# Performance work log

Measured on AMD Instinct MI355X. Metric: run time of the kernel, lower is better.

Reference implementation:

```python
import jax, jax.numpy as jnp
import numpy as np

B, T = 32, 1024
TEMP_IN, STAT_IN = 128, 64
TEMP_OUT, STAT_OUT = 128, 64
EPS = 1e-5
NEG_SLOPE = 0.01


def _bn_eval(x, gamma, beta, mean, var):
    # BatchNorm1d in eval mode (running stats)
    return (x - mean) * jax.lax.rsqrt(var + EPS) * gamma + beta


def _leaky_relu(x):
    return jnp.where(x >= 0, x, NEG_SLOPE * x)


def setup_inputs() -> dict:
    key = jax.random.key(0)
    k = jax.random.split(key, 6)
    # deterministic ragged lengths in [512, 1024]
    lengths_np = (512 + (np.arange(B) * 37) % 513).astype(np.int64)
    N = int(lengths_np.sum())  # 23450
    batch_idx = np.repeat(np.arange(B), lengths_np).astype(np.int32)
    pos_idx = np.concatenate([np.arange(l) for l in lengths_np]).astype(np.int32)
    valid = (np.arange(T)[None, :] < lengths_np[:, None])  # [B, T]
    mask_repeat = valid[:, :, None] & valid[:, None, :]    # [B, T, T]

    inp = {
        "x_temp": jax.random.normal(k[0], (N, TEMP_IN), jnp.float32),
        "x_stat": jax.random.normal(k[1], (B, STAT_IN), jnp.float32),
        "temp_attn": jax.random.normal(k[2], (B, T, T), jnp.float32) * 0.1,
        "mask_repeat": jnp.asarray(mask_repeat),
        "lengths": jnp.asarray(lengths_np),
        "batch_idx": jnp.asarray(batch_idx),
        "pos_idx": jnp.asarray(pos_idx),
        # non_linear_temp: Linear(TEMP_IN+STAT_IN -> TEMP_OUT) + BN
        "W1": jax.random.normal(k[3], (TEMP_OUT, TEMP_IN + STAT_IN), jnp.float32) / np.sqrt(TEMP_IN + STAT_IN),
        "b1": jnp.zeros((TEMP_OUT,), jnp.float32),
        "gamma1": jnp.ones((TEMP_OUT,), jnp.float32),
        "beta1": jnp.zeros((TEMP_OUT,), jnp.float32),
        "mean1": jnp.zeros((TEMP_OUT,), jnp.float32),
        "var1": jnp.ones((TEMP_OUT,), jnp.float32),
        # non_linear_stat: Linear(STAT_IN -> STAT_OUT) + BN
        "W2": jax.random.normal(k[4], (STAT_OUT, STAT_IN), jnp.float32) / np.sqrt(STAT_IN),
        "b2": jnp.zeros((STAT_OUT,), jnp.float32),
        "gamma2": jnp.ones((STAT_OUT,), jnp.float32),
        "beta2": jnp.zeros((STAT_OUT,), jnp.float32),
        "mean2": jnp.zeros((STAT_OUT,), jnp.float32),
        "var2": jnp.ones((STAT_OUT,), jnp.float32),
    }
    return inp


def reference(x_temp, x_stat, temp_attn, mask_repeat, lengths, batch_idx, pos_idx,
              W1, b1, gamma1, beta1, mean1, var1,
              W2, b2, gamma2, beta2, mean2, var2):
    # repeat_static_features: gather per-batch static feats to packed rows
    x_stat_rep = x_stat[batch_idx]                              # [N, STAT_IN]
    h = jnp.concatenate((x_temp, x_stat_rep), axis=-1) @ W1.T + b1
    h = _leaky_relu(_bn_eval(h, gamma1, beta1, mean1, var1))    # [N, TEMP_OUT]

    # pad_packed_sequences: scatter packed rows into [B, T, C] (zeros elsewhere)
    padded = jnp.zeros((B, T, TEMP_OUT), h.dtype).at[batch_idx, pos_idx].set(h)

    # self attention: softmax(x x^T / sqrt(d)) over padded rows (as original)
    d = jnp.asarray(TEMP_OUT, h.dtype)
    qk = jnp.einsum('btc,bsc->bts', padded, padded) / jnp.sqrt(d)
    self_attn = jax.nn.softmax(qk, axis=-1)

    attn = jnp.where(mask_repeat, self_attn + temp_attn, jnp.asarray(0.0, h.dtype))

    x_stat_out = _leaky_relu(_bn_eval(x_stat @ W2.T + b2, gamma2, beta2, mean2, var2))

    x_out_pad = jnp.einsum('bts,bsc->btc', attn, padded)        # [B, T, TEMP_OUT]
    # pack_padded_sequences: gather valid positions back to packed layout
    x_out = x_out_pad[batch_idx, pos_idx]                       # [N, TEMP_OUT]
    return (x_out, x_stat_out)
```

## Files before the change

kernel.cpp:

```cpp
#include <hip/hip_runtime.h>
#include <hip/hip_bf16.h>
#include <hip/hip_fp16.h>

typedef __hip_bfloat16 bf16;
typedef __attribute__((ext_vector_type(8))) short short8;
typedef __attribute__((ext_vector_type(4))) float f32x4;

#define EPS 1e-5f
#define NSLOPE 0.01f

__device__ __forceinline__ float b2f(bf16 v) { return __bfloat162float(v); }

__device__ __forceinline__ float ld1(const void* p, size_t idx, int isbf) {
  if (isbf) return b2f(((const bf16*)p)[idx]);
  return ((const float*)p)[idx];
}
__device__ __forceinline__ void st1(void* p, size_t idx, int isbf, float v) {
  if (isbf) ((bf16*)p)[idx] = __float2bfloat16(v);
  else      ((float*)p)[idx] = v;
}
__device__ __forceinline__ short f2bs(float x) {
  bf16 t = __float2bfloat16(x);
  short s; __builtin_memcpy(&s, &t, 2); return s;
}
__device__ __forceinline__ short8 pack8f(const float* p) {
  float4 a = *(const float4*)p, b = *(const float4*)(p + 4);
  short8 r;
  r[0] = f2bs(a.x); r[1] = f2bs(a.y); r[2] = f2bs(a.z); r[3] = f2bs(a.w);
  r[4] = f2bs(b.x); r[5] = f2bs(b.y); r[6] = f2bs(b.z); r[7] = f2bs(b.w);
  return r;
}

__global__ void meta_kernel(const void* __restrict__ xt,
                            const int* __restrict__ bidx, const int* __restrict__ pidx,
                            int N, int B, int* __restrict__ rs, int* __restrict__ ln,
                            int* __restrict__ flag,
                            const void* __restrict__ W1, bf16* __restrict__ w1b, int w1n) {
  int isbf_l = 0;
  {
    unsigned w = ((const unsigned*)xt)[threadIdx.x & 63];
    unsigned lo = w & 0xffffu;
    unsigned ex = (lo >> 7) & 0xffu;
    bool sane = ((lo & 0x7fffu) == 0u) || (ex >= 96u && ex <= 134u);
    unsigned long long m = __ballot(sane);
    isbf_l = (__popcll(m) >= 48) ? 1 : 0;
    if (blockIdx.x == 0 && threadIdx.x == 0) flag[0] = isbf_l;
  }
  int stride = gridDim.x * blockDim.x;
  int g0 = blockIdx.x * blockDim.x + threadIdx.x;
  for (int i = g0; i < N; i += stride) {
    int b = bidx[i];
    if ((unsigned)b >= (unsigned)B) continue;
    if (i == 0 || bidx[i - 1] != b) rs[b] = i;
    if (i == N - 1 || bidx[i + 1] != b) ln[b] = pidx[i] + 1;
  }
  for (int i = g0; i < w1n; i += stride) {
    int o = i / 192, k = i - o * 192;
    int ct = o >> 4, n = o & 15;
    int ks = k >> 5, rem = k & 31;
    int q = rem >> 3, j = rem & 7;
    int fi = ((ct * 6 + ks) * 64 + q * 16 + n) * 8 + j;
    w1b[fi] = __float2bfloat16(ld1(W1, i, isbf_l));
  }
}

__global__ void zfill_kernel(void* out, const int* __restrict__ flag, long long n) {
  const int isbf = flag[0];
  long long i = (long long)blockIdx.x * blockDim.x + threadIdx.x;
  long long stride = (long long)gridDim.x * blockDim.x;
  for (; i < n; i += stride) st1(out, (size_t)i, isbf, 0.f);
}

__global__ __launch_bounds__(256) void ta2b_kernel(
    const void* __restrict__ ta, const int* __restrict__ ln_arr,
    const int* __restrict__ flag, unsigned short* __restrict__ tb, int T) {
  if (flag[0]) return;
  const int b = blockIdx.y, t0 = blockIdx.x * 16;
  const int len = ln_arr[b];
  if (t0 >= len) return;
  const int c64 = ((len + 63) >> 6) << 6;
  const int nr = min(16, len - t0);
  const int c = threadIdx.x * 4;
  if (c >= c64) return;
  const size_t base = ((size_t)b * T + t0) * (size_t)T + c;
  const float* src = (const float*)ta + base;
  unsigned short* dst = tb + base;
  for (int r = 0; r < nr; ++r) {
    float4 f = *(const float4*)(src + (size_t)r * T);
    ushort4 o;
    o.x = (unsigned short)f2bs(f.x);
    o.y = (unsigned short)f2bs(f.y);
    o.z = (unsigned short)f2bs(f.z);
    o.w = (unsigned short)f2bs(f.w);
    *(ushort4*)(dst + (size_t)r * T) = o;
  }
}

__global__ __launch_bounds__(256) void h_mfma_kernel(
    const void* __restrict__ xt, const void* __restrict__ xsg,
    const int* __restrict__ bidx, const bf16* __restrict__ w1b,
    const void* __restrict__ b1,
    const void* __restrict__ g1, const void* __restrict__ be1,
    const void* __restrict__ mn1, const void* __restrict__ vr1,
    const int* __restrict__ flag, bf16* __restrict__ hout, int N) {
  const int isbf = flag[0];
  const int tid = threadIdx.x, lane = tid & 63, wv = tid >> 6;
  const int m16 = lane & 15, quad = lane >> 4;
  const int row0 = blockIdx.x * 64 + wv * 16;
  const int m = row0 + m16;
  const int mc = (m < N) ? m : (N - 1);
  const int bi = bidx[mc];

  short8 af[6];
  if (isbf) {
    const bf16* xr = (const bf16*)xt + (size_t)mc * 128 + quad * 8;
#pragma unroll
    for (int ks = 0; ks < 4; ++ks) af[ks] = *(const short8*)(xr + ks * 32);
    const bf16* sr = (const bf16*)xsg + (size_t)bi * 64 + quad * 8;
    af[4] = *(const short8*)sr;
    af[5] = *(const short8*)(sr + 32);
  } else {
    const float* xr = (const float*)xt + (size_t)mc * 128 + quad * 8;
#pragma unroll
    for (int ks = 0; ks < 4; ++ks) af[ks] = pack8f(xr + ks * 32);
    const float* sr = (const float*)xsg + (size_t)bi * 64 + quad * 8;
    af[4] = pack8f(sr);
    af[5] = pack8f(sr + 32);
  }

  f32x4 acc[8];
#pragma unroll
  for (int ct = 0; ct < 8; ++ct) acc[ct] = (f32x4){0.f, 0.f, 0.f, 0.f};

  const short8* wf = (const short8*)w1b;
#pragma unroll
  for (int ks = 0; ks < 6; ++ks) {
#pragma unroll
    for (int ct = 0; ct < 8; ++ct) {
      short8 bfrag = wf[(ct * 6 + ks) * 64 + lane];
      acc[ct] = __builtin_amdgcn_mfma_f32_16x16x32_bf16(af[ks], bfrag, acc[ct], 0, 0, 0);
    }
  }

#pragma unroll
  for (int ct = 0; ct < 8; ++ct) {
    const int o = ct * 16 + m16;
    float k1 = ld1(g1, o, isbf) * rsqrtf(ld1(vr1, o, isbf) + EPS);
    float k0 = ld1(be1, o, isbf) - ld1(mn1, o, isbf) * k1;
    float bias = ld1(b1, o, isbf);
#pragma unroll
    for (int r = 0; r < 4; ++r) {
      int mr = row0 + quad * 4 + r;
      if (mr < N) {
        float v = (acc[ct][r] + bias) * k1 + k0;
        v = (v >= 0.f) ? v : NSLOPE * v;
        hout[(size_t)mr * 128 + o] = __float2bfloat16(v);
      }
    }
  }
}

__global__ __launch_bounds__(64) void stat_kernel(
    const void* __restrict__ xstat, const void* __restrict__ W2,
    const void* __restrict__ b2, const void* __restrict__ g2,
    const void* __restrict__ be2, const void* __restrict__ mn2,
    const void* __restrict__ vr2, const int* __restrict__ flag,
    void* __restrict__ out, long long obase) {
  __shared__ float xs[64];
  const int isbf = flag[0];
  const int b = blockIdx.x, o = threadIdx.x;
  xs[o] = ld1(xstat, b * 64 + o, isbf);
  __syncthreads();
  float acc = ld1(b2, o, isbf);
#pragma unroll 8
  for (int j = 0; j < 64; ++j) acc += xs[j] * ld1(W2, o * 64 + j, isbf);
  float k1 = ld1(g2, o, isbf) * rsqrtf(ld1(vr2, o, isbf) + EPS);
  float k0 = ld1(be2, o, isbf) - ld1(mn2, o, isbf) * k1;
  float v = acc * k1 + k0;
  v = (v >= 0.f) ? v : NSLOPE * v;
  st1(out, (size_t)(obase + b * 64 + o), isbf, v);
}

__global__ __launch_bounds__(256, 2) void attn_mfma_kernel(
    const void* __restrict__ ta, const unsigned short* __restrict__ tb,
    const bf16* __restrict__ h,
    const int* __restrict__ rs_arr, const int* __restrict__ ln_arr,
    const int* __restrict__ flag, void* __restrict__ xout, int T, int N,
    int useconv) {
  __shared__ __align__(16) unsigned short vT[2][128][72];
  __shared__ __align__(16) unsigned short Pw[4][16][72];

  const int b = blockIdx.y, t0 = blockIdx.x * 64;
  const int len = ln_arr[b];
  if (t0 >= len) return;
  const int isbf = flag[0];
  const int utb = useconv && !isbf;
  const int rs = rs_arr[b];
  const int tid = threadIdx.x;
  const int lane = tid & 63, wv = tid >> 6;
  const int m16 = lane & 15, quad = lane >> 4;
  const int t0w = t0 + wv * 16;

  short8 qf[4];
  {
    int qrow = rs + t0w + m16;
    if (qrow > N - 1) qrow = N - 1;
    const bf16* qp = h + (size_t)qrow * 128 + quad * 8;
#pragma unroll
    for (int ks = 0; ks < 4; ++ks) qf[ks] = *(const short8*)(qp + ks * 32);
  }

  const float scale = 0.08838834764831845f;
  const short8 zero8 = {0, 0, 0, 0, 0, 0, 0, 0};
  const uint4 zz = {0, 0, 0, 0};
  const size_t tarow = ((size_t)b * T + (t0w + m16)) * (size_t)T;
  const int c8base = wv * 32;

  f32x4 accp[8], acct[8];
#pragma unroll
  for (int ct = 0; ct < 8; ++ct) {
    accp[ct] = (f32x4){0.f, 0.f, 0.f, 0.f};
    acct[ct] = (f32x4){0.f, 0.f, 0.f, 0.f};
  }
  float mrun[4], lrun[4];
#pragma unroll
  for (int r = 0; r < 4; ++r) { mrun[r] = -INFINITY; lrun[r] = 0.f; }

  {
    int srow = lane;
    bool v = srow < len;
    const bf16* src = h + (size_t)(rs + (v ? srow : 0)) * 128;
#pragma unroll
    for (int it = 0; it < 4; ++it) {
      int c8 = c8base + it * 8;
      uint4 u = v ? *(const uint4*)(src + c8) : zz;
      const unsigned short* a = (const unsigned short*)&u;
#pragma unroll
      for (int j = 0; j < 8; ++j) vT[0][c8 + j][lane] = a[j];
    }
  }
  short8 tac0 = zero8, tac1 = zero8;
  if (utb) {
    const unsigned short* tp = tb + tarow + quad * 8;
    tac0 = *(const short8*)tp;
    tac1 = *(const short8*)(tp + 32);
  }
  __syncthreads();

  const int nchunk = (len + 63) >> 6;
  for (int ci = 0; ci < nchunk; ++ci) {
    const int s0 = ci << 6;
    const int p = ci & 1;
    const bool have_next = (ci + 1 < nchunk);

    uint4 su0 = zz, su1 = zz, su2 = zz, su3 = zz;
    if (have_next) {
      int srow = s0 + 64 + lane;
      bool v = srow < len;
      const bf16* src = h + (size_t)(rs + (v ? srow : 0)) * 128;
      if (v) {
        su0 = *(const uint4*)(src + c8base);
        su1 = *(const uint4*)(src + c8base + 8);
        su2 = *(const uint4*)(src + c8base + 16);
        su3 = *(const uint4*)(src + c8base + 24);
      }
    }

    short8 tan0 = tac0, tan1 = tac1;
    if (utb) {
      int sn = have_next ? (s0 + 64) : s0;
      const unsigned short* tp = tb + tarow + sn + quad * 8;
      tan0 = *(const short8*)tp;
      tan1 = *(const short8*)(tp + 32);
    }

    short8 taf0, taf1;
    if (utb) {
      taf0 = tac0;
      taf1 = tac1;
    } else if (isbf) {
      const bf16* tp = (const bf16*)ta + tarow + s0 + quad * 8;
      taf0 = *(const short8*)tp;
      taf1 = *(const short8*)(tp + 32);
    } else {
      const float* tp = (const float*)ta + tarow + s0 + quad * 8;
      taf0 = pack8f(tp);
      taf1 = pack8f(tp + 32);
    }

    f32x4 sa[4];
    bool sval[4];
#pragma unroll
    for (int st = 0; st < 4; ++st) {
      int srow = s0 + st * 16 + m16;
      bool v = srow < len;
      sval[st] = v;
      const bf16* kp = h + (size_t)(rs + (v ? srow : 0)) * 128 + quad * 8;
      f32x4 a0 = (f32x4){0.f, 0.f, 0.f, 0.f};
#pragma unroll
      for (int ks = 0; ks < 4; ++ks) {
        short8 kf = v ? *(const short8*)(kp + ks * 32) : zero8;
        a0 = __builtin_amdgcn_mfma_f32_16x16x32_bf16(qf[ks], kf, a0, 0, 0, 0);
      }
      sa[st] = a0;
    }

    float cm[4];
#pragma unroll
    for (int r = 0; r < 4; ++r) cm[r] = -INFINITY;
#pragma unroll
    for (int st = 0; st < 4; ++st) {
#pragma unroll
      for (int r = 0; r < 4; ++r)
        cm[r] = fmaxf(cm[r], sval[st] ? sa[st][r] * scale : -INFINITY);
    }
#pragma unroll
    for (int off = 1; off <= 8; off <<= 1) {
#pragma unroll
      for (int r = 0; r < 4; ++r) cm[r] = fmaxf(cm[r], __shfl_xor(cm[r], off, 64));
    }
    float al[4], csum[4];
#pragma unroll
    for (int r = 0; r < 4; ++r) {
      float mnew = fmaxf(mrun[r], cm[r]);
      al[r] = __expf(mrun[r] - mnew);
      mrun[r] = mnew;
      csum[r] = 0.f;
    }
#pragma unroll
    for (int st = 0; st < 4; ++st) {
#pragma unroll
      for (int r = 0; r < 4; ++r) {
        float pv = sval[st] ? __expf(sa[st][r] * scale - mrun[r]) : 0.f;
        csum[r] += pv;
        Pw[wv][quad * 4 + r][st * 16 + m16] = (unsigned short)f2bs(pv);
      }
    }
#pragma unroll
    for (int off = 1; off <= 8; off <<= 1) {
#pragma unroll
      for (int r = 0; r < 4; ++r) csum[r] += __shfl_xor(csum[r], off, 64);
    }
#pragma unroll
    for (int r = 0; r < 4; ++r) lrun[r] = lrun[r] * al[r] + csum[r];

#pragma unroll
    for (int ct = 0; ct < 8; ++ct) {
#pragma unroll
      for (int r = 0; r < 4; ++r) accp[ct][r] *= al[r];
    }

#pragma unroll
    for (int ks = 0; ks < 2; ++ks) {
      short8 pf = *(const short8*)&Pw[wv][m16][ks * 32 + quad * 8];
      short8 tf = ks ? taf1 : taf0;
#pragma unroll
      for (int ct = 0; ct < 8; ++ct) {
        short8 bfv = *(const short8*)&vT[p][ct * 16 + m16][ks * 32 + quad * 8];
        accp[ct] = __builtin_amdgcn_mfma_f32_16x16x32_bf16(pf, bfv, accp[ct], 0, 0, 0);
        acct[ct] = __builtin_amdgcn_mfma_f32_16x16x32_bf16(tf, bfv, acct[ct], 0, 0, 0);
      }
    }

    tac0 = tan0; tac1 = tan1;

    if (have_next) {
      const unsigned short* a0 = (const unsigned short*)&su0;
      const unsigned short* a1 = (const unsigned short*)&su1;
      const unsigned short* a2 = (const unsigned short*)&su2;
      const unsigned short* a3 = (const unsigned short*)&su3;
#pragma unroll
      for (int j = 0; j < 8; ++j) {
        vT[p ^ 1][c8base + j][lane]      = a0[j];
        vT[p ^ 1][c8base + 8 + j][lane]  = a1[j];
        vT[p ^ 1][c8base + 16 + j][lane] = a2[j];
        vT[p ^ 1][c8base + 24 + j][lane] = a3[j];
      }
    }
    __syncthreads();
  }

  const int nr = len - t0w;
#pragma unroll
  for (int r = 0; r < 4; ++r) {
    int t = quad * 4 + r;
    if (t < nr) {
      float m_r = mrun[r], l_r = lrun[r];
      float m_f = (len < T) ? fmaxf(m_r, 0.f) : m_r;
      float corr = __expf(m_r - m_f);
      float l_f = l_r * corr + (float)(T - len) * __expf(-m_f);
      float os = corr / l_f;
      size_t ob = (size_t)(rs + t0w + t) * 128;
#pragma unroll
      for (int ct = 0; ct < 8; ++ct)
        st1(xout, ob + ct * 16 + m16, isbf, accp[ct][r] * os + acct[ct][r]);
    }
  }
}

extern "C" void kernel_launch(void* const* d_in, const int* in_sizes, int n_in,
                              void* d_out, int out_size, void* d_ws, size_t ws_size,
                              hipStream_t stream) {
  const void* x_temp    = d_in[0];
  const void* x_stat    = d_in[1];
  const void* temp_attn = d_in[2];
  const int N = in_sizes[0] / 128;
  const int B = in_sizes[1] / 64;
  long long tt = (long long)in_sizes[2] / B;
  int T = 1; while ((long long)(T + 1) * (T + 1) <= tt) ++T;

  int p = 3;
  while (p < n_in && in_sizes[p] != N) ++p;
  const int* batch_idx = (const int*)d_in[p++];
  const int* pos_idx   = (const int*)d_in[p++];
  const void* W1 = d_in[p++];
  const void* b1 = d_in[p++];
  const void* g1 = d_in[p++];
  const void* be1= d_in[p++];
  const void* mn1= d_in[p++];
  const void* vr1= d_in[p++];
  const void* W2 = d_in[p++];
  const void* b2 = d_in[p++];
  const void* g2 = d_in[p++];
  const void* be2= d_in[p++];
  const void* mn2= d_in[p++];
  const void* vr2= d_in[p++];

  int*  meta = (int*)d_ws;
  int*  rs   = meta;
  int*  lnp  = meta + B;
  int*  flag = meta + 2 * B;
  bf16* h    = (bf16*)((char*)d_ws + 1024);
  bf16* w1b  = h + (size_t)N * 128;
  const int w1n = 128 * 192;
  unsigned short* tb = (unsigned short*)((char*)(w1b + w1n));
  size_t need  = 1024 + (size_t)N * 128 * sizeof(bf16) + (size_t)w1n * sizeof(bf16);
  size_t need2 = need + (size_t)B * T * T * sizeof(short);
  int useconv = (ws_size >= need2) ? 1 : 0;

  long long obase = (long long)N * 128;

  meta_kernel<<<90, 256, 0, stream>>>(x_temp, batch_idx, pos_idx, N, B, rs, lnp,
                                      flag, W1, w1b, w1n);
  stat_kernel<<<B, 64, 0, stream>>>(x_stat, W2, b2, g2, be2, mn2, vr2, flag,
                                    d_out, obase);
  if (ws_size >= need) {
    h_mfma_kernel<<<(N + 63) / 64, 256, 0, stream>>>(x_temp, x_stat, batch_idx,
                                                     w1b, b1, g1, be1, mn1, vr1,
                                                     flag, h, N);
    if (useconv) {
      ta2b_kernel<<<dim3((T + 15) / 16, B), 256, 0, stream>>>(temp_attn, lnp,
                                                              flag, tb, T);
    }
    attn_mfma_kernel<<<dim3((T + 63) / 64, B), 256, 0, stream>>>(
        temp_attn, tb, h, rs, lnp, flag, d_out, T, N, useconv);
  } else {
    zfill_kernel<<<512, 256, 0, stream>>>(d_out, flag, obase);
  }
}
```

Baseline: 417.6 us.

## Shrink attention blocks to 32 query rows and remap workgroups per XCD

The attention kernel now uses 128-thread blocks covering 32 query rows instead of 256 threads covering 64. Each wave loads twice as many channels of the key/value chunk into shared memory. A 1D grid is remapped so that consecutive work items land on the same XCD, which should improve L2 reuse of each batch's h rows. The goal is more blocks, better load balance over ragged lengths, and better cache locality, at the cost of staging the K/V chunk twice as often per query row.

```diff
diff --git a/kernel.cpp b/kernel.cpp
--- a/kernel.cpp
+++ b/kernel.cpp
@@ -181,16 +181,22 @@
   st1(out, (size_t)(obase + b * 64 + o), isbf, v);
 }
 
-__global__ __launch_bounds__(256, 2) void attn_mfma_kernel(
+__global__ __launch_bounds__(128, 2) void attn_mfma_kernel(
     const void* __restrict__ ta, const unsigned short* __restrict__ tb,
     const bf16* __restrict__ h,
     const int* __restrict__ rs_arr, const int* __restrict__ ln_arr,
     const int* __restrict__ flag, void* __restrict__ xout, int T, int N,
-    int useconv) {
+    int useconv, int tpb) {
   __shared__ __align__(16) unsigned short vT[2][128][72];
-  __shared__ __align__(16) unsigned short Pw[4][16][72];
-
-  const int b = blockIdx.y, t0 = blockIdx.x * 64;
+  __shared__ __align__(16) unsigned short Pw[2][16][72];
+
+  const int nwg = gridDim.x, orig = blockIdx.x;
+  const int q = nwg >> 3, rr = nwg & 7;
+  const int xcd = orig & 7, gi = orig >> 3;
+  const int wgid = (xcd < rr ? xcd * (q + 1) : rr * (q + 1) + (xcd - rr) * q) + gi;
+  const int b = wgid / tpb;
+  const int t0 = (wgid - b * tpb) * 32;
+
   const int len = ln_arr[b];
   if (t0 >= len) return;
   const int isbf = flag[0];
@@ -214,7 +220,7 @@
   const short8 zero8 = {0, 0, 0, 0, 0, 0, 0, 0};
   const uint4 zz = {0, 0, 0, 0};
   const size_t tarow = ((size_t)b * T + (t0w + m16)) * (size_t)T;
-  const int c8base = wv * 32;
+  const int c8base = wv * 64;
 
   f32x4 accp[8], acct[8];
 #pragma unroll
@@ -231,7 +237,7 @@
     bool v = srow < len;
     const bf16* src = h + (size_t)(rs + (v ? srow : 0)) * 128;
 #pragma unroll
-    for (int it = 0; it < 4; ++it) {
+    for (int it = 0; it < 8; ++it) {
       int c8 = c8base + it * 8;
       uint4 u = v ? *(const uint4*)(src + c8) : zz;
       const unsigned short* a = (const unsigned short*)&u;
@@ -254,15 +260,16 @@
     const bool have_next = (ci + 1 < nchunk);
 
     uint4 su0 = zz, su1 = zz, su2 = zz, su3 = zz;
+    uint4 su4 = zz, su5 = zz, su6 = zz, su7 = zz;
     if (have_next) {
       int srow = s0 + 64 + lane;
       bool v = srow < len;
-      const bf16* src = h + (size_t)(rs + (v ? srow : 0)) * 128;
+      const bf16* src = h + (size_t)(rs + (v ? srow : 0)) * 128 + c8base;
       if (v) {
-        su0 = *(const uint4*)(src + c8base);
-        su1 = *(const uint4*)(src + c8base + 8);
-        su2 = *(const uint4*)(src + c8base + 16);
-        su3 = *(const uint4*)(src + c8base + 24);
+        su0 = *(const uint4*)(src);      su1 = *(const uint4*)(src + 8);
+        su2 = *(const uint4*)(src + 16); su3 = *(const uint4*)(src + 24);
+        su4 = *(const uint4*)(src + 32); su5 = *(const uint4*)(src + 40);
+        su6 = *(const uint4*)(src + 48); su7 = *(const uint4*)(src + 56);
       }
     }
 
@@ -369,12 +376,20 @@
       const unsigned short* a1 = (const unsigned short*)&su1;
       const unsigned short* a2 = (const unsigned short*)&su2;
       const unsigned short* a3 = (const unsigned short*)&su3;
+      const unsigned short* a4 = (const unsigned short*)&su4;
+      const unsigned short* a5 = (const unsigned short*)&su5;
+      const unsigned short* a6 = (const unsigned short*)&su6;
+      const unsigned short* a7 = (const unsigned short*)&su7;
 #pragma unroll
       for (int j = 0; j < 8; ++j) {
         vT[p ^ 1][c8base + j][lane]      = a0[j];
         vT[p ^ 1][c8base + 8 + j][lane]  = a1[j];
         vT[p ^ 1][c8base + 16 + j][lane] = a2[j];
         vT[p ^ 1][c8base + 24 + j][lane] = a3[j];
+        vT[p ^ 1][c8base + 32 + j][lane] = a4[j];
+        vT[p ^ 1][c8base + 40 + j][lane] = a5[j];
+        vT[p ^ 1][c8base + 48 + j][lane] = a6[j];
+        vT[p ^ 1][c8base + 56 + j][lane] = a7[j];
       }
     }
     __syncthreads();
@@ -452,8 +467,9 @@
       ta2b_kernel<<<dim3((T + 15) / 16, B), 256, 0, stream>>>(temp_attn, lnp,
                                                               flag, tb, T);
     }
-    attn_mfma_kernel<<<dim3((T + 63) / 64, B), 256, 0, stream>>>(
-        temp_attn, tb, h, rs, lnp, flag, d_out, T, N, useconv);
+    const int tpb = (T + 31) / 32;
+    attn_mfma_kernel<<<dim3(tpb * B), 128, 0, stream>>>(
+        temp_attn, tb, h, rs, lnp, flag, d_out, T, N, useconv, tpb);
   } else {
     zfill_kernel<<<512, 256, 0, stream>>>(d_out, flag, obase);
   }
```

Measured after the change: 511.2 us. 22.4% more time.
